# Kernel optimization log

Hardware: AMD Instinct MI355X
Metric: run time of the kernel (lower is better)

Reference implementation:

```python
import jax, jax.numpy as jnp
import numpy as np

B, H, W, C = 4, 128, 128, 256
HEADS, DHEAD = 8, 32


def conv2d(x, w, b=None, groups=1, pad=0):
    # x: [N,C,H,W], w: [O, C//groups, kh, kw]
    out = jax.lax.conv_general_dilated(
        x, w, window_strides=(1, 1), padding=[(pad, pad), (pad, pad)],
        dimension_numbers=("NCHW", "OIHW", "NCHW"), feature_group_count=groups)
    if b is not None:
        out = out + b[None, :, None, None]
    return out


def setup_inputs() -> dict:
    key = jax.random.key(0)
    ks = jax.random.split(key, 16)
    g = lambda i, shape, s=0.02: jax.random.normal(ks[i], shape, jnp.float32) * s
    return {
        "x": jax.random.normal(ks[0], (B, H, W, C), jnp.float32),
        "mask": jax.random.uniform(ks[1], (1, C, H, W), jnp.float32),
        "wq": g(2, (C, C)),
        "wk": g(3, (C, C)),
        "wv": g(4, (C, C)),
        "rescale": jnp.ones((HEADS, 1, 1), jnp.float32),
        "wproj": g(5, (C, C)),
        "bproj": jnp.zeros((C,), jnp.float32),
        "mg_w1": g(6, (C, C, 1, 1)),
        "mg_b1": jnp.zeros((C,), jnp.float32),
        "mg_w2": g(7, (C, C, 1, 1)),
        "mg_b2": jnp.zeros((C,), jnp.float32),
        "mg_dw": g(8, (C, 1, 5, 5)),
        "mg_db": jnp.zeros((C,), jnp.float32),
        "be_w1": g(9, (C, 1, 3, 3)),
        "be_w2": g(10, (C, 1, 3, 3)),
    }


def _l2norm(t, axis):
    n = jnp.sqrt(jnp.sum(t * t, axis=axis, keepdims=True))
    return t / jnp.maximum(n, 1e-12)


def reference(x, mask, wq, wk, wv, rescale, wproj, bproj,
              mg_w1, mg_b1, mg_w2, mg_b2, mg_dw, mg_db, be_w1, be_w2):
    b, h, w, c = x.shape
    heads = rescale.shape[0]
    d = c // heads
    n = h * w

    xf = x.reshape(b, n, c)
    q_inp = xf @ wq   # [b,n,c]
    k_inp = xf @ wk
    v_inp = xf @ wv

    # MaskGuidedMechanism (h==w so shift_back is identity)
    m = conv2d(mask, mg_w1, mg_b1)                                   # [1,c,h,w]
    attn_map = jax.nn.sigmoid(conv2d(conv2d(m, mg_w2, mg_b2), mg_dw, mg_db, groups=c, pad=2))
    m = m * attn_map + m
    mask_emb = jnp.transpose(m, (0, 2, 3, 1))                        # [1,h,w,c]
    ma = jnp.broadcast_to(mask_emb, (b, h, w, c)).reshape(b, n, c)

    split = lambda t: t.reshape(b, n, heads, d).transpose(0, 2, 1, 3)  # [b,heads,n,d]
    q, k, v, ma = map(split, (q_inp, k_inp, v_inp, ma))
    v = v * ma

    # channel attention: normalize over token dim n
    qn = _l2norm(q, axis=2)
    kn = _l2norm(k, axis=2)
    attn = jnp.einsum("bhni,bhnj->bhij", kn, qn)                     # [b,heads,d,d]
    attn = jax.nn.softmax(attn * rescale, axis=-1)
    out = jnp.einsum("bhij,bhnj->bhin", attn, v)                     # [b,heads,d,n]

    out = out.transpose(0, 3, 1, 2).reshape(b, n, heads * d)         # [b,n,c]
    out_c = (out @ wproj + bproj).reshape(b, h, w, c)

    # band_emb: depthwise3x3 -> GELU(exact) -> depthwise3x3 on v_inp image
    v_img = v_inp.reshape(b, h, w, c).transpose(0, 3, 1, 2)          # [b,c,h,w]
    y = conv2d(v_img, be_w1, groups=c, pad=1)
    y = jax.nn.gelu(y, approximate=False)
    y = conv2d(y, be_w2, groups=c, pad=1)
    out_p = y.transpose(0, 2, 3, 1)

    return out_c + out_p
```

## Files before the change

kernel.cpp:

```cpp
#include <hip/hip_runtime.h>
#include <stdint.h>

#define B 4
#define HW 128
#define C 256
#define NTOK 16384
#define MALL 65536
#define HEADS 8
#define DH 32

typedef float f32x4 __attribute__((ext_vector_type(4)));
typedef short s16x8 __attribute__((ext_vector_type(8)));
typedef short s16x4 __attribute__((ext_vector_type(4)));
typedef __bf16 bf16x8 __attribute__((ext_vector_type(8)));

__device__ __forceinline__ float bf2f(unsigned short u) {
  union { unsigned int i; float f; } x;
  x.i = ((unsigned int)u) << 16;
  return x.f;
}
__device__ __forceinline__ unsigned short f2bf(float f) {
  union { float f; unsigned int i; } x;
  x.f = f;
  unsigned int lsb = (x.i >> 16) & 1u;
  unsigned int r = x.i + 0x7fffu + lsb;
  return (unsigned short)(r >> 16);
}

__device__ __forceinline__ void gload_lds16(const void* g, void* l) {
  auto gp = reinterpret_cast<const __attribute__((address_space(1))) unsigned int*>(
      reinterpret_cast<uintptr_t>(g));
  auto lp = reinterpret_cast<__attribute__((address_space(3))) unsigned int*>(
      reinterpret_cast<uintptr_t>(l));
  __builtin_amdgcn_global_load_lds(gp, lp, 16, 0, 0);
}

#define CFENCE asm volatile("" ::: "memory")
#define RAWBAR()                      \
  do {                                \
    CFENCE;                           \
    __builtin_amdgcn_s_barrier();     \
    CFENCE;                           \
  } while (0)
#define LDSBAR()                                        \
  do {                                                  \
    asm volatile("s_waitcnt lgkmcnt(0)" ::: "memory");  \
    __builtin_amdgcn_s_barrier();                       \
    CFENCE;                                             \
  } while (0)

__global__ __launch_bounds__(256) void cast_x_kernel(const float* __restrict__ x,
                                                     unsigned short* __restrict__ xb) {
  const size_t stride = (size_t)gridDim.x * blockDim.x * 4;
  for (size_t i = ((size_t)blockIdx.x * blockDim.x + threadIdx.x) * 4; i < (size_t)MALL * C;
       i += stride) {
    const float4 v = *(const float4*)&x[i];
    s16x4 o;
    o[0] = (short)f2bf(v.x);
    o[1] = (short)f2bf(v.y);
    o[2] = (short)f2bf(v.z);
    o[3] = (short)f2bf(v.w);
    *(s16x4*)&xb[i] = o;
  }
}

__global__ __launch_bounds__(256) void prep_w_kernel(
    const float* __restrict__ wq, const float* __restrict__ wk, const float* __restrict__ wv,
    const float* __restrict__ wproj, const float* __restrict__ w1, const float* __restrict__ w2,
    unsigned short* __restrict__ wqkvT, unsigned short* __restrict__ wprojT,
    unsigned short* __restrict__ w1b, unsigned short* __restrict__ w2b) {
  const int idx = blockIdx.x * 256 + threadIdx.x;
  const int mat = blockIdx.y;
  const int n = idx >> 8, k = idx & 255;
  switch (mat) {
    case 0: wqkvT[idx] = f2bf(wq[k * 256 + n]); break;
    case 1: wqkvT[65536 + idx] = f2bf(wk[k * 256 + n]); break;
    case 2: wqkvT[131072 + idx] = f2bf(wv[k * 256 + n]); break;
    case 3: wprojT[idx] = f2bf(wproj[k * 256 + n]); break;
    case 4: w1b[idx] = f2bf(w1[idx]); break;
    case 5: w2b[idx] = f2bf(w2[idx]); break;
  }
}

__global__ __launch_bounds__(1024) void tmask_kernel(const float* __restrict__ mask,
                                                     unsigned short* __restrict__ mT) {
  __shared__ float tile[32][33];
  const int p0 = blockIdx.x * 32, c0 = blockIdx.y * 32;
  const int tx = threadIdx.x & 31, ty = threadIdx.x >> 5;
  tile[ty][tx] = mask[(size_t)(c0 + ty) * NTOK + p0 + tx];
  __syncthreads();
  mT[(size_t)(p0 + ty) * C + c0 + tx] = f2bf(tile[tx][ty]);
}

__global__ __launch_bounds__(512) void gemm_bt256_kernel(
    const unsigned short* __restrict__ A, const unsigned short* __restrict__ Bt,
    const int nbn, const int mode, unsigned short* __restrict__ ob0,
    unsigned short* __restrict__ ob1, unsigned short* __restrict__ ob2,
    const float* __restrict__ bias, float* __restrict__ of32,
    const unsigned short* __restrict__ y2) {
  __shared__ unsigned short smem[49152];
  unsigned short* lAb = smem;
  unsigned short* lBb = smem + 24576;
  const int nwg = gridDim.x;
  const int bid = blockIdx.x;
  const int qd = nwg >> 3, rr = nwg & 7;
  const int xcd = bid & 7, sidx = bid >> 3;
  const int swz = (xcd < rr ? xcd * (qd + 1) : rr * (qd + 1) + (xcd - rr) * qd) + sidx;
  const int m0 = (swz / nbn) * 256;
  const int n0 = (swz % nbn) * 256;
  const int t = threadIdx.x;
  const int w = t >> 6, l = t & 63;
  const int wr = w >> 2, wc = w & 3;
  const int lr = l & 15, lg = l >> 4;

  const int srow = t >> 2;
  const int ssl = (t & 3) ^ ((t >> 3) & 3);

  auto stageA = [&](int kt) {
    unsigned short* d = lAb + (kt % 3) * 8192;
    const size_t kb = ((size_t)kt * 32 + ssl * 8) * 2;
    gload_lds16((const char*)A + ((size_t)(m0 + srow) * 256) * 2 + kb, (char*)d + t * 16);
    gload_lds16((const char*)A + ((size_t)(m0 + 128 + srow) * 256) * 2 + kb,
                (char*)d + 8192 + t * 16);
  };
  auto stageB = [&](int kt) {
    unsigned short* d = lBb + (kt % 3) * 8192;
    const size_t kb = ((size_t)kt * 32 + ssl * 8) * 2;
    gload_lds16((const char*)Bt + ((size_t)(n0 + srow) * 256) * 2 + kb, (char*)d + t * 16);
    gload_lds16((const char*)Bt + ((size_t)(n0 + 128 + srow) * 256) * 2 + kb,
                (char*)d + 8192 + t * 16);
  };

  f32x4 acc[8][4];
#pragma unroll
  for (int m = 0; m < 8; ++m)
#pragma unroll
    for (int j = 0; j < 4; ++j) acc[m][j] = f32x4{0.f, 0.f, 0.f, 0.f};

  const int asl = (lg ^ ((lr >> 1) & 3)) * 8;
  const int aoff = lr * 32 + asl;
  const int awb = wr * 4096;
  const int boff = (wc >> 1) * 4096 + ((wc & 1) * 64 + lr) * 32 + asl;

  stageA(0); stageB(0); stageA(1); stageB(1);
  asm volatile("s_waitcnt vmcnt(4)" ::: "memory");
  RAWBAR();

#pragma unroll
  for (int kt = 0; kt < 8; ++kt) {
    const unsigned short* bufA = lAb + (kt % 3) * 8192;
    const unsigned short* bufB = lBb + (kt % 3) * 8192;
    bf16x8 bfr[4], af[4];
#pragma unroll
    for (int j = 0; j < 4; ++j) bfr[j] = *(const bf16x8*)&bufB[boff + j * 512];
#pragma unroll
    for (int m = 0; m < 4; ++m) af[m] = *(const bf16x8*)&bufA[awb + aoff + m * 512];
    if (kt < 6) stageA(kt + 2);
    RAWBAR();
    __builtin_amdgcn_s_setprio(1);
#pragma unroll
    for (int m = 0; m < 4; ++m)
#pragma unroll
      for (int j = 0; j < 4; ++j)
        acc[m][j] = __builtin_amdgcn_mfma_f32_16x16x32_bf16(af[m], bfr[j], acc[m][j], 0, 0, 0);
    __builtin_amdgcn_s_setprio(0);
    RAWBAR();
#pragma unroll
    for (int m = 0; m < 4; ++m) af[m] = *(const bf16x8*)&bufA[awb + aoff + (m + 4) * 512];
    if (kt < 6) stageB(kt + 2);
    RAWBAR();
    __builtin_amdgcn_s_setprio(1);
#pragma unroll
    for (int m = 0; m < 4; ++m)
#pragma unroll
      for (int j = 0; j < 4; ++j)
        acc[m + 4][j] =
            __builtin_amdgcn_mfma_f32_16x16x32_bf16(af[m], bfr[j], acc[m + 4][j], 0, 0, 0);
    __builtin_amdgcn_s_setprio(0);
    if (kt < 6) asm volatile("s_waitcnt vmcnt(4)" ::: "memory");
    else asm volatile("s_waitcnt vmcnt(0)" ::: "memory");
    RAWBAR();
  }

  if (mode == 0) {
    unsigned short* dst = (n0 < 256) ? ob0 : (n0 < 512 ? ob1 : ob2);
    unsigned short* eph = smem;
#pragma unroll
    for (int h = 0; h < 2; ++h) {
      LDSBAR();
#pragma unroll
      for (int mm = 0; mm < 4; ++mm) {
        const int m = h * 4 + mm;
        const int lrow = wr * 64 + mm * 16 + lg * 4;
#pragma unroll
        for (int j = 0; j < 4; ++j) {
          const int col = wc * 64 + j * 16 + lr;
#pragma unroll
          for (int r = 0; r < 4; ++r) eph[(lrow + r) * 264 + col] = f2bf(acc[m][j][r]);
        }
      }
      LDSBAR();
      const int col16 = t & 31;
#pragma unroll
      for (int c2 = 0; c2 < 8; ++c2) {
        const int lrow = c2 * 16 + (t >> 5);
        const int grow = m0 + (lrow >> 6) * 128 + h * 64 + (lrow & 63);
        const s16x8 v = *(const s16x8*)&eph[lrow * 264 + col16 * 8];
        *(s16x8*)&dst[(size_t)grow * C + col16 * 8] = v;
      }
    }
  } else {
    float* ephf = (float*)smem;
    const int colc = t & 63;
    const f32x4 bv = *(const f32x4*)&bias[colc * 4];
#pragma unroll
    for (int qtr = 0; qtr < 4; ++qtr) {
      LDSBAR();
#pragma unroll
      for (int mm = 0; mm < 2; ++mm) {
        const int m = qtr * 2 + mm;
        const int lrow = wr * 32 + mm * 16 + lg * 4;
#pragma unroll
        for (int j = 0; j < 4; ++j) {
          const int col = wc * 64 + j * 16 + lr;
#pragma unroll
          for (int r = 0; r < 4; ++r) ephf[(lrow + r) * 260 + col] = acc[m][j][r];
        }
      }
      LDSBAR();
#pragma unroll
      for (int c2 = 0; c2 < 8; ++c2) {
        const int lrow = c2 * 8 + (t >> 6);
        const int grow = m0 + (lrow >> 5) * 128 + qtr * 32 + (lrow & 31);
        const f32x4 v = *(const f32x4*)&ephf[lrow * 260 + colc * 4];
        const s16x4 yv = *(const s16x4*)&y2[(size_t)grow * C + colc * 4];
        f32x4 o;
#pragma unroll
        for (int e = 0; e < 4; ++e) o[e] = v[e] + bv[e] + bf2f((unsigned short)yv[e]);
        *(f32x4*)&of32[(size_t)grow * C + colc * 4] = o;
      }
    }
  }
}

__global__ __launch_bounds__(256) void gemm_bt_kernel(
    const unsigned short* __restrict__ A, const unsigned short* __restrict__ Bt, const int K,
    const int nbn, const int mode, unsigned short* __restrict__ ob0,
    unsigned short* __restrict__ ob1, unsigned short* __restrict__ ob2,
    const float* __restrict__ bias, float* __restrict__ of32) {
  __shared__ unsigned short lA[2][128 * 64];
  __shared__ unsigned short lB[2][128 * 64];
  const int nwg = gridDim.x;
  const int bid = blockIdx.x;
  const int qd = nwg >> 3, rr = nwg & 7;
  const int xcd = bid & 7, sidx = bid >> 3;
  const int swz = (xcd < rr ? xcd * (qd + 1) : rr * (qd + 1) + (xcd - rr) * qd) + sidx;
  const int m0 = (swz / nbn) * 128;
  const int n0 = (swz % nbn) * 128;
  const int t = threadIdx.x;
  const int w = t >> 6, l = t & 63;
  const int wr = w >> 1, wc = w & 1;
  const int lr = l & 15, lg = l >> 4;

  const int strow = (l >> 3);
  const int scolb = (((l & 7) ^ strow) << 4);

  f32x4 acc[4][4];
#pragma unroll
  for (int i = 0; i < 4; ++i)
#pragma unroll
    for (int j = 0; j < 4; ++j) acc[i][j] = f32x4{0.f, 0.f, 0.f, 0.f};

  auto stage = [&](int buf, int k0) {
#pragma unroll
    for (int s = 0; s < 4; ++s) {
      const int seg = w * 4 + s;
      const int row = seg * 8 + strow;
      gload_lds16((const char*)A + ((size_t)(m0 + row) * K + k0) * 2 + scolb,
                  (char*)&lA[buf][0] + seg * 1024 + (l & 7) * 16);
      gload_lds16((const char*)Bt + ((size_t)(n0 + row) * K + k0) * 2 + scolb,
                  (char*)&lB[buf][0] + seg * 1024 + (l & 7) * 16);
    }
  };
  auto compute = [&](int buf) {
#pragma unroll
    for (int kk = 0; kk < 64; kk += 32) {
      bf16x8 af[4], bfr[4];
      const int sbase = (kk >> 3) + lg;
      const int p = (sbase ^ (lr & 7)) << 3;
#pragma unroll
      for (int i = 0; i < 4; ++i)
        af[i] = *(const bf16x8*)&lA[buf][(wr * 64 + i * 16 + lr) * 64 + p];
#pragma unroll
      for (int j = 0; j < 4; ++j)
        bfr[j] = *(const bf16x8*)&lB[buf][(wc * 64 + j * 16 + lr) * 64 + p];
#pragma unroll
      for (int i = 0; i < 4; ++i)
#pragma unroll
        for (int j = 0; j < 4; ++j)
          acc[i][j] = __builtin_amdgcn_mfma_f32_16x16x32_bf16(af[i], bfr[j], acc[i][j], 0, 0, 0);
    }
  };

  stage(0, 0);
  __syncthreads();
  int cur = 0;
  for (int k0 = 64; k0 < K; k0 += 64) {
    stage(cur ^ 1, k0);
    compute(cur);
    __syncthreads();
    cur ^= 1;
  }
  compute(cur);

#pragma unroll
  for (int i = 0; i < 4; ++i) {
    const int grow = m0 + wr * 64 + i * 16 + lg * 4;
#pragma unroll
    for (int j = 0; j < 4; ++j) {
      const int gcol = n0 + wc * 64 + j * 16 + lr;
#pragma unroll
      for (int r = 0; r < 4; ++r) {
        const float v = acc[i][j][r];
        const size_t row = (size_t)(grow + r);
        if (mode == 0) {
          unsigned short* dst = (gcol < 256) ? ob0 : (gcol < 512 ? ob1 : ob2);
          dst[row * C + (gcol & 255)] = f2bf(v);
        } else if (mode == 1) {
          ob0[row * C + gcol] = f2bf(v + bias[gcol]);
        } else {
          const size_t idx = row * C + gcol;
          of32[idx] += v + bias[gcol];
        }
      }
    }
  }
}

__global__ __launch_bounds__(256) void mask_dw5_kernel(
    const unsigned short* __restrict__ m2, const unsigned short* __restrict__ m1,
    const float* __restrict__ dw, const float* __restrict__ db,
    unsigned short* __restrict__ memb) {
  __shared__ float wlds[25 * 256];
  __shared__ float blds[256];
  const int t = threadIdx.x;
  const int y = blockIdx.y;
  const int x0 = blockIdx.x * 16 + (t >> 6) * 4;
  const int cg = (t & 63) * 4;
#pragma unroll
  for (int e = 0; e < 25; ++e) wlds[e * 256 + t] = dw[t * 25 + e];
  blds[t] = db[t];
  __syncthreads();

  const f32x4 bias = *(const f32x4*)&blds[cg];
  f32x4 acc[4];
#pragma unroll
  for (int xi = 0; xi < 4; ++xi) acc[xi] = bias;

#pragma unroll
  for (int dy = 0; dy < 5; ++dy) {
    const int yy = y + dy - 2;
    if (yy < 0 || yy >= HW) continue;
    f32x4 col[8];
#pragma unroll
    for (int j = 0; j < 8; ++j) {
      const int xx = x0 - 2 + j;
      if (xx >= 0 && xx < HW) {
        const s16x4 v = *(const s16x4*)&m2[((size_t)yy * HW + xx) * C + cg];
        col[j][0] = bf2f((unsigned short)v[0]);
        col[j][1] = bf2f((unsigned short)v[1]);
        col[j][2] = bf2f((unsigned short)v[2]);
        col[j][3] = bf2f((unsigned short)v[3]);
      } else {
        col[j] = f32x4{0.f, 0.f, 0.f, 0.f};
      }
    }
#pragma unroll
    for (int dx = 0; dx < 5; ++dx) {
      const f32x4 wv = *(const f32x4*)&wlds[(dy * 5 + dx) * 256 + cg];
#pragma unroll
      for (int xi = 0; xi < 4; ++xi) acc[xi] += wv * col[dx + xi];
    }
  }

#pragma unroll
  for (int xi = 0; xi < 4; ++xi) {
    const size_t oi = ((size_t)y * HW + x0 + xi) * C + cg;
    const s16x4 mv = *(const s16x4*)&m1[oi];
    s16x4 o;
#pragma unroll
    for (int ch = 0; ch < 4; ++ch) {
      const float a = 1.f / (1.f + __expf(-acc[xi][ch]));
      o[ch] = (short)f2bf(bf2f((unsigned short)mv[ch]) * (1.f + a));
    }
    *(s16x4*)&memb[oi] = o;
  }
}

__global__ __launch_bounds__(256) void gram_kernel(const unsigned short* __restrict__ qb,
                                                   const unsigned short* __restrict__ kb,
                                                   float* __restrict__ Gpart,
                                                   float* __restrict__ ssq,
                                                   float* __restrict__ ssk) {
  const int chunk = blockIdx.x;
  const int h = blockIdx.y;
  const int b = blockIdx.z;
  __shared__ unsigned short lk[128 * 32], lq[128 * 32];
  const int t = threadIdx.x;
  const int wv = t >> 6;
  const int i0 = (t & 7) * 4, j0 = ((t >> 3) & 7) * 4;
  const int lrow = t >> 2, lcb = (t & 3) * 8;
  float acc[4][4] = {};
  float sq[8] = {}, sk[8] = {};
  for (int sub = 0; sub < 8; ++sub) {
    const size_t nbase = (size_t)b * NTOK + chunk * 1024 + sub * 128;
    __syncthreads();
#pragma unroll
    for (int it = 0; it < 2; ++it) {
      const int row = it * 64 + lrow;
      const s16x8 kv8 = *(const s16x8*)&kb[(nbase + row) * C + h * 32 + lcb];
      const s16x8 qv8 = *(const s16x8*)&qb[(nbase + row) * C + h * 32 + lcb];
      *(s16x8*)&lk[row * 32 + lcb] = kv8;
      *(s16x8*)&lq[row * 32 + lcb] = qv8;
#pragma unroll
      for (int e = 0; e < 8; ++e) {
        const float kf = bf2f((unsigned short)kv8[e]);
        sk[e] += kf * kf;
        const float qf = bf2f((unsigned short)qv8[e]);
        sq[e] += qf * qf;
      }
    }
    __syncthreads();
    for (int n = wv; n < 128; n += 4) {
      s16x4 kv = *(const s16x4*)&lk[n * 32 + i0];
      s16x4 qv = *(const s16x4*)&lq[n * 32 + j0];
      float kf[4], qf[4];
#pragma unroll
      for (int e = 0; e < 4; ++e) {
        kf[e] = bf2f((unsigned short)kv[e]);
        qf[e] = bf2f((unsigned short)qv[e]);
      }
#pragma unroll
      for (int a = 0; a < 4; ++a)
#pragma unroll
        for (int bb = 0; bb < 4; ++bb) acc[a][bb] += kf[a] * qf[bb];
    }
  }
  const int pc = chunk * 4 + wv;
  float* dst = Gpart + (((size_t)pc * B + b) * HEADS + h) * 1024;
#pragma unroll
  for (int a = 0; a < 4; ++a)
#pragma unroll
    for (int bb = 0; bb < 4; ++bb) dst[(i0 + a) * 32 + (j0 + bb)] = acc[a][bb];
  __syncthreads();
  float* fq = (float*)lq;
  float* fk = (float*)lk;
#pragma unroll
  for (int e = 0; e < 8; ++e) {
    fq[t * 8 + e] = sq[e];
    fk[t * 8 + e] = sk[e];
  }
  __syncthreads();
  if (t < 32) {
    const int tm = t >> 3, e = t & 7;
    float s1 = 0.f, s2 = 0.f;
    for (int k2 = 0; k2 < 64; ++k2) {
      const int tt = tm + k2 * 4;
      s1 += fq[tt * 8 + e];
      s2 += fk[tt * 8 + e];
    }
    ssq[((size_t)b * 16 + chunk) * C + h * 32 + t] = s1;
    ssk[((size_t)b * 16 + chunk) * C + h * 32 + t] = s2;
  }
}

__global__ __launch_bounds__(256) void softmax_kernel(
    const float* __restrict__ Gpart, const float* __restrict__ ssq,
    const float* __restrict__ ssk, const float* __restrict__ rescale,
    unsigned short* __restrict__ attnb) {
  const int h = blockIdx.x, b = blockIdx.y;
  const int t = threadIdx.x;
  __shared__ float G[1024];
  __shared__ float nq[32], nk[32];
#pragma unroll
  for (int e = 0; e < 4; ++e) {
    const int cell = e * 256 + t;
    float s = 0.f;
    for (int pc = 0; pc < 64; ++pc)
      s += Gpart[(((size_t)pc * B + b) * HEADS + h) * 1024 + cell];
    G[cell] = s;
  }
  if (t < 64) {
    const int d = t & 31;
    const float* ss = (t < 32) ? ssq : ssk;
    float s = 0.f;
    for (int ch = 0; ch < 16; ++ch) s += ss[((size_t)b * 16 + ch) * C + h * 32 + d];
    const float nn = fmaxf(sqrtf(s), 1e-12f);
    if (t < 32) nq[d] = nn;
    else nk[d] = nn;
  }
  __syncthreads();
  if (t < 32) {
    const int i = t;
    const float rs = rescale[h];
    float row[32];
    float mx = -1e30f;
#pragma unroll
    for (int j = 0; j < 32; ++j) {
      const float v = G[i * 32 + j] / (nk[i] * nq[j]) * rs;
      row[j] = v;
      mx = fmaxf(mx, v);
    }
    float sum = 0.f;
#pragma unroll
    for (int j = 0; j < 32; ++j) {
      const float e = expf(row[j] - mx);
      row[j] = e;
      sum += e;
    }
    const float inv = 1.f / sum;
#pragma unroll
    for (int j = 0; j < 32; ++j)
      attnb[(((size_t)b * HEADS + h) * 32 + i) * 32 + j] = f2bf(row[j] * inv);
  }
}

#define PVP 264
#define ATP 40
__global__ __launch_bounds__(256) void pv_kernel(const unsigned short* __restrict__ vb,
                                                 const unsigned short* __restrict__ memb,
                                                 const unsigned short* __restrict__ attnb,
                                                 unsigned short* __restrict__ outp) {
  const int n0 = blockIdx.x * 64;
  const int b = blockIdx.y;
  __shared__ unsigned short vma[64 * PVP];
  __shared__ unsigned short at[HEADS * 32 * ATP];
  const int t = threadIdx.x, w = t >> 6, l = t & 63;
  const int lr = l & 15, lg = l >> 4;
  for (int e = t; e < 8192; e += 256) {
    const int h = e >> 10, ij = e & 1023;
    at[(h * 32 + (ij >> 5)) * ATP + (ij & 31)] = attnb[(size_t)b * 8192 + e];
  }
  {
    const int row = t >> 2, cs = (t & 3) * 64;
#pragma unroll
    for (int i2 = 0; i2 < 8; ++i2) {
      const int c = cs + i2 * 8;
      s16x8 vv = *(const s16x8*)&vb[((size_t)b * NTOK + n0 + row) * C + c];
      s16x8 mm = *(const s16x8*)&memb[(size_t)(n0 + row) * C + c];
      s16x8 o;
#pragma unroll
      for (int e = 0; e < 8; ++e)
        o[e] = (short)f2bf(bf2f((unsigned short)vv[e]) * bf2f((unsigned short)mm[e]));
      *(s16x8*)&vma[row * PVP + c] = o;
    }
  }
  __syncthreads();
  f32x4 acc[4][4];
#pragma unroll
  for (int i = 0; i < 4; ++i)
#pragma unroll
    for (int j = 0; j < 4; ++j) acc[i][j] = f32x4{0.f, 0.f, 0.f, 0.f};
#pragma unroll
  for (int j = 0; j < 4; ++j) {
    const int head = w * 2 + (j >> 1);
    const int colh = (j & 1) * 16 + lr;
    const bf16x8 bfr = *(const bf16x8*)&at[(head * 32 + colh) * ATP + lg * 8];
#pragma unroll
    for (int i = 0; i < 4; ++i) {
      const bf16x8 af = *(const bf16x8*)&vma[(i * 16 + lr) * PVP + head * 32 + lg * 8];
      acc[i][j] = __builtin_amdgcn_mfma_f32_16x16x32_bf16(af, bfr, acc[i][j], 0, 0, 0);
    }
  }
#pragma unroll
  for (int i = 0; i < 4; ++i) {
#pragma unroll
    for (int j = 0; j < 4; ++j) {
      const int head = w * 2 + (j >> 1);
      const int gcol = head * 32 + (j & 1) * 16 + lr;
      const int grow = n0 + i * 16 + lg * 4;
#pragma unroll
      for (int r = 0; r < 4; ++r)
        outp[((size_t)b * NTOK + grow + r) * C + gcol] = f2bf(acc[i][j][r]);
    }
  }
}

__global__ __launch_bounds__(512) void dw3_kernel(const unsigned short* __restrict__ in,
                                                  const float* __restrict__ wgt,
                                                  unsigned short* __restrict__ out_bf,
                                                  float* __restrict__ out_f32,
                                                  const int do_gelu, const int write_f32) {
  const int y = blockIdx.x;
  const int b = blockIdx.y;
  const int t = threadIdx.x;
  const int cg = (t & 63) * 4;
  const int x0 = (t >> 6) * 16;
  float w[9][4];
#pragma unroll
  for (int e = 0; e < 9; ++e)
#pragma unroll
    for (int ch = 0; ch < 4; ++ch) w[e][ch] = wgt[(cg + ch) * 9 + e];
  const int ym = y - 1, yp = y + 1;
  const bool hm = (ym >= 0), hp = (yp < HW);
  const size_t base = (size_t)b * NTOK * C + cg;
  auto ld4 = [&](int yy, int xx) -> f32x4 {
    const s16x4 v = *(const s16x4*)&in[base + ((size_t)yy * HW + xx) * C];
    f32x4 f;
    f[0] = bf2f((unsigned short)v[0]);
    f[1] = bf2f((unsigned short)v[1]);
    f[2] = bf2f((unsigned short)v[2]);
    f[3] = bf2f((unsigned short)v[3]);
    return f;
  };
  const f32x4 zero = {0.f, 0.f, 0.f, 0.f};
  f32x4 a0, a1, a2, b0, b1, b2;
  if (x0 > 0) {
    a0 = hm ? ld4(ym, x0 - 1) : zero;
    a1 = ld4(y, x0 - 1);
    a2 = hp ? ld4(yp, x0 - 1) : zero;
  } else {
    a0 = a1 = a2 = zero;
  }
  b0 = hm ? ld4(ym, x0) : zero;
  b1 = ld4(y, x0);
  b2 = hp ? ld4(yp, x0) : zero;
  for (int xi = 0; xi < 16; ++xi) {
    const int x = x0 + xi;
    f32x4 c0, c1, c2;
    if (x + 1 < HW) {
      c0 = hm ? ld4(ym, x + 1) : zero;
      c1 = ld4(y, x + 1);
      c2 = hp ? ld4(yp, x + 1) : zero;
    } else {
      c0 = c1 = c2 = zero;
    }
    float res[4];
#pragma unroll
    for (int ch = 0; ch < 4; ++ch) {
      float r = w[0][ch] * a0[ch] + w[1][ch] * b0[ch] + w[2][ch] * c0[ch] +
                w[3][ch] * a1[ch] + w[4][ch] * b1[ch] + w[5][ch] * c1[ch] +
                w[6][ch] * a2[ch] + w[7][ch] * b2[ch] + w[8][ch] * c2[ch];
      if (do_gelu) r = 0.5f * r * (1.f + erff(r * 0.70710678118654752f));
      res[ch] = r;
    }
    const size_t oi = base + ((size_t)y * HW + x) * C;
    if (write_f32) {
      const f32x4 o = {res[0], res[1], res[2], res[3]};
      *(f32x4*)&out_f32[oi] = o;
    } else {
      s16x4 o;
      o[0] = (short)f2bf(res[0]);
      o[1] = (short)f2bf(res[1]);
      o[2] = (short)f2bf(res[2]);
      o[3] = (short)f2bf(res[3]);
      *(s16x4*)&out_bf[oi] = o;
    }
    a0 = b0; a1 = b1; a2 = b2;
    b0 = c0; b1 = c1; b2 = c2;
  }
}

extern "C" void kernel_launch(void* const* d_in, const int* in_sizes, int n_in, void* d_out,
                              int out_size, void* d_ws, size_t ws_size, hipStream_t stream) {
  (void)in_sizes; (void)n_in; (void)out_size; (void)ws_size;
  const float* x = (const float*)d_in[0];
  const float* maskp = (const float*)d_in[1];
  const float* wq = (const float*)d_in[2];
  const float* wk = (const float*)d_in[3];
  const float* wv = (const float*)d_in[4];
  const float* rescale = (const float*)d_in[5];
  const float* wproj = (const float*)d_in[6];
  const float* bproj = (const float*)d_in[7];
  const float* mg_w1 = (const float*)d_in[8];
  const float* mg_b1 = (const float*)d_in[9];
  const float* mg_w2 = (const float*)d_in[10];
  const float* mg_b2 = (const float*)d_in[11];
  const float* mg_dw = (const float*)d_in[12];
  const float* mg_db = (const float*)d_in[13];
  const float* be_w1 = (const float*)d_in[14];
  const float* be_w2 = (const float*)d_in[15];
  float* out = (float*)d_out;
  char* ws = (char*)d_ws;

  unsigned short* xb = (unsigned short*)(ws + 0ull);
  unsigned short* qb = (unsigned short*)(ws + 33554432ull);
  unsigned short* kb = (unsigned short*)(ws + 67108864ull);
  unsigned short* vb = (unsigned short*)(ws + 100663296ull);
  unsigned short* mT = (unsigned short*)(ws + 134217728ull);
  unsigned short* m1b = (unsigned short*)(ws + 142606336ull);
  unsigned short* m2b = (unsigned short*)(ws + 150994944ull);
  unsigned short* wqkvT = (unsigned short*)(ws + 159383552ull);
  unsigned short* wprojT = (unsigned short*)(ws + 159776768ull);
  unsigned short* w1b = (unsigned short*)(ws + 159907840ull);
  unsigned short* w2b = (unsigned short*)(ws + 160038912ull);
  float* ssq = (float*)(ws + 160169984ull);
  float* ssk = (float*)(ws + 160432128ull);
  unsigned short* attnb = (unsigned short*)(ws + 160694272ull);
  float* Gpart = (float*)m2b;
  unsigned short* memb = mT;
  unsigned short* outpre = xb;
  unsigned short* y1 = qb;
  unsigned short* y2 = kb;

  cast_x_kernel<<<2048, 256, 0, stream>>>(x, xb);
  prep_w_kernel<<<dim3(256, 6), 256, 0, stream>>>(wq, wk, wv, wproj, mg_w1, mg_w2, wqkvT,
                                                  wprojT, w1b, w2b);
  tmask_kernel<<<dim3(512, 8), 1024, 0, stream>>>(maskp, mT);
  gemm_bt_kernel<<<256, 256, 0, stream>>>(mT, w1b, 256, 2, 1, m1b, nullptr, nullptr, mg_b1,
                                          nullptr);
  gemm_bt_kernel<<<256, 256, 0, stream>>>(m1b, w2b, 256, 2, 1, m2b, nullptr, nullptr, mg_b2,
                                          nullptr);
  mask_dw5_kernel<<<dim3(8, 128), 256, 0, stream>>>(m2b, m1b, mg_dw, mg_db, memb);
  gemm_bt256_kernel<<<768, 512, 0, stream>>>(xb, wqkvT, 3, 0, qb, kb, vb, nullptr, nullptr,
                                             nullptr);
  gram_kernel<<<dim3(16, 8, 4), 256, 0, stream>>>(qb, kb, Gpart, ssq, ssk);
  softmax_kernel<<<dim3(8, 4), 256, 0, stream>>>(Gpart, ssq, ssk, rescale, attnb);
  pv_kernel<<<dim3(256, 4), 256, 0, stream>>>(vb, memb, attnb, outpre);
  dw3_kernel<<<dim3(128, 4), 512, 0, stream>>>(vb, be_w1, y1, nullptr, 1, 0);
  dw3_kernel<<<dim3(128, 4), 512, 0, stream>>>(y1, be_w2, y2, nullptr, 0, 0);
  gemm_bt256_kernel<<<256, 512, 0, stream>>>(outpre, wprojT, 1, 2, nullptr, nullptr, nullptr,
                                             bproj, out, y2);
}
```

Before: 299.6 us.

## Shrink GEMM LDS to double buffering and chunk epilogue per wave row

The 256x256 GEMM kernel moves from a three-stage LDS ring to two buffers, staging A and B for the next k-step together and waiting for all loads each iteration. The epilogue staging is split into smaller per-wave-row chunks so it fits the reduced 64 KB shared buffer. The aim is to lower LDS use per block, possibly allowing two blocks per CU and cutting per-iteration barriers. The cost is less prefetch depth, since a full vmcnt(0) wait each iteration exposes load latency, and the epilogue needs more barrier rounds.

Result: no change. 298.4 us (-0.4%).

```diff
diff --git a/kernel.cpp b/kernel.cpp
--- a/kernel.cpp
+++ b/kernel.cpp
@@ -98,9 +98,9 @@
     unsigned short* __restrict__ ob1, unsigned short* __restrict__ ob2,
     const float* __restrict__ bias, float* __restrict__ of32,
     const unsigned short* __restrict__ y2) {
-  __shared__ unsigned short smem[49152];
+  __shared__ alignas(16) unsigned short smem[32768];
   unsigned short* lAb = smem;
-  unsigned short* lBb = smem + 24576;
+  unsigned short* lBb = smem + 16384;
   const int nwg = gridDim.x;
   const int bid = blockIdx.x;
   const int qd = nwg >> 3, rr = nwg & 7;
@@ -117,14 +117,14 @@
   const int ssl = (t & 3) ^ ((t >> 3) & 3);
 
   auto stageA = [&](int kt) {
-    unsigned short* d = lAb + (kt % 3) * 8192;
+    unsigned short* d = lAb + (kt & 1) * 8192;
     const size_t kb = ((size_t)kt * 32 + ssl * 8) * 2;
     gload_lds16((const char*)A + ((size_t)(m0 + srow) * 256) * 2 + kb, (char*)d + t * 16);
     gload_lds16((const char*)A + ((size_t)(m0 + 128 + srow) * 256) * 2 + kb,
                 (char*)d + 8192 + t * 16);
   };
   auto stageB = [&](int kt) {
-    unsigned short* d = lBb + (kt % 3) * 8192;
+    unsigned short* d = lBb + (kt & 1) * 8192;
     const size_t kb = ((size_t)kt * 32 + ssl * 8) * 2;
     gload_lds16((const char*)Bt + ((size_t)(n0 + srow) * 256) * 2 + kb, (char*)d + t * 16);
     gload_lds16((const char*)Bt + ((size_t)(n0 + 128 + srow) * 256) * 2 + kb,
@@ -142,43 +142,36 @@
   const int awb = wr * 4096;
   const int boff = (wc >> 1) * 4096 + ((wc & 1) * 64 + lr) * 32 + asl;
 
-  stageA(0); stageB(0); stageA(1); stageB(1);
-  asm volatile("s_waitcnt vmcnt(4)" ::: "memory");
+  stageA(0); stageB(0);
+  asm volatile("s_waitcnt vmcnt(0)" ::: "memory");
   RAWBAR();
 
 #pragma unroll
   for (int kt = 0; kt < 8; ++kt) {
-    const unsigned short* bufA = lAb + (kt % 3) * 8192;
-    const unsigned short* bufB = lBb + (kt % 3) * 8192;
-    bf16x8 bfr[4], af[4];
+    const unsigned short* bufA = lAb + (kt & 1) * 8192;
+    const unsigned short* bufB = lBb + (kt & 1) * 8192;
+    bf16x8 bfr[4], af[4], af2[4];
 #pragma unroll
     for (int j = 0; j < 4; ++j) bfr[j] = *(const bf16x8*)&bufB[boff + j * 512];
 #pragma unroll
     for (int m = 0; m < 4; ++m) af[m] = *(const bf16x8*)&bufA[awb + aoff + m * 512];
-    if (kt < 6) stageA(kt + 2);
-    RAWBAR();
+#pragma unroll
+    for (int m = 0; m < 4; ++m) af2[m] = *(const bf16x8*)&bufA[awb + aoff + (m + 4) * 512];
+    if (kt < 7) { stageA(kt + 1); stageB(kt + 1); }
     __builtin_amdgcn_s_setprio(1);
 #pragma unroll
     for (int m = 0; m < 4; ++m)
 #pragma unroll
       for (int j = 0; j < 4; ++j)
         acc[m][j] = __builtin_amdgcn_mfma_f32_16x16x32_bf16(af[m], bfr[j], acc[m][j], 0, 0, 0);
-    __builtin_amdgcn_s_setprio(0);
-    RAWBAR();
-#pragma unroll
-    for (int m = 0; m < 4; ++m) af[m] = *(const bf16x8*)&bufA[awb + aoff + (m + 4) * 512];
-    if (kt < 6) stageB(kt + 2);
-    RAWBAR();
-    __builtin_amdgcn_s_setprio(1);
 #pragma unroll
     for (int m = 0; m < 4; ++m)
 #pragma unroll
       for (int j = 0; j < 4; ++j)
         acc[m + 4][j] =
-            __builtin_amdgcn_mfma_f32_16x16x32_bf16(af[m], bfr[j], acc[m + 4][j], 0, 0, 0);
+            __builtin_amdgcn_mfma_f32_16x16x32_bf16(af2[m], bfr[j], acc[m + 4][j], 0, 0, 0);
     __builtin_amdgcn_s_setprio(0);
-    if (kt < 6) asm volatile("s_waitcnt vmcnt(4)" ::: "memory");
-    else asm volatile("s_waitcnt vmcnt(0)" ::: "memory");
+    if (kt < 7) asm volatile("s_waitcnt vmcnt(0)" ::: "memory");
     RAWBAR();
   }
 
@@ -186,25 +179,27 @@
     unsigned short* dst = (n0 < 256) ? ob0 : (n0 < 512 ? ob1 : ob2);
     unsigned short* eph = smem;
 #pragma unroll
-    for (int h = 0; h < 2; ++h) {
+    for (int c = 0; c < 4; ++c) {
       LDSBAR();
-#pragma unroll
-      for (int mm = 0; mm < 4; ++mm) {
-        const int m = h * 4 + mm;
-        const int lrow = wr * 64 + mm * 16 + lg * 4;
-#pragma unroll
-        for (int j = 0; j < 4; ++j) {
-          const int col = wc * 64 + j * 16 + lr;
-#pragma unroll
-          for (int r = 0; r < 4; ++r) eph[(lrow + r) * 264 + col] = f2bf(acc[m][j][r]);
+      if (wr == (c >> 1)) {
+#pragma unroll
+        for (int mm = 0; mm < 4; ++mm) {
+          const int m = (c & 1) * 4 + mm;
+          const int lrow = mm * 16 + lg * 4;
+#pragma unroll
+          for (int j = 0; j < 4; ++j) {
+            const int col = wc * 64 + j * 16 + lr;
+#pragma unroll
+            for (int r = 0; r < 4; ++r) eph[(lrow + r) * 264 + col] = f2bf(acc[m][j][r]);
+          }
         }
       }
       LDSBAR();
       const int col16 = t & 31;
 #pragma unroll
-      for (int c2 = 0; c2 < 8; ++c2) {
+      for (int c2 = 0; c2 < 4; ++c2) {
         const int lrow = c2 * 16 + (t >> 5);
-        const int grow = m0 + (lrow >> 6) * 128 + h * 64 + (lrow & 63);
+        const int grow = m0 + c * 64 + lrow;
         const s16x8 v = *(const s16x8*)&eph[lrow * 264 + col16 * 8];
         *(s16x8*)&dst[(size_t)grow * C + col16 * 8] = v;
       }
@@ -214,24 +209,26 @@
     const int colc = t & 63;
     const f32x4 bv = *(const f32x4*)&bias[colc * 4];
 #pragma unroll
-    for (int qtr = 0; qtr < 4; ++qtr) {
+    for (int c = 0; c < 8; ++c) {
       LDSBAR();
-#pragma unroll
-      for (int mm = 0; mm < 2; ++mm) {
-        const int m = qtr * 2 + mm;
-        const int lrow = wr * 32 + mm * 16 + lg * 4;
-#pragma unroll
-        for (int j = 0; j < 4; ++j) {
-          const int col = wc * 64 + j * 16 + lr;
-#pragma unroll
-          for (int r = 0; r < 4; ++r) ephf[(lrow + r) * 260 + col] = acc[m][j][r];
+      if (wr == (c >> 2)) {
+#pragma unroll
+        for (int mm = 0; mm < 2; ++mm) {
+          const int m = (c & 3) * 2 + mm;
+          const int lrow = mm * 16 + lg * 4;
+#pragma unroll
+          for (int j = 0; j < 4; ++j) {
+            const int col = wc * 64 + j * 16 + lr;
+#pragma unroll
+            for (int r = 0; r < 4; ++r) ephf[(lrow + r) * 260 + col] = acc[m][j][r];
+          }
         }
       }
       LDSBAR();
 #pragma unroll
-      for (int c2 = 0; c2 < 8; ++c2) {
+      for (int c2 = 0; c2 < 4; ++c2) {
         const int lrow = c2 * 8 + (t >> 6);
-        const int grow = m0 + (lrow >> 5) * 128 + qtr * 32 + (lrow & 31);
+        const int grow = m0 + c * 32 + lrow;
         const f32x4 v = *(const f32x4*)&ephf[lrow * 260 + colc * 4];
         const s16x4 yv = *(const s16x4*)&y2[(size_t)grow * C + colc * 4];
         f32x4 o;
```
